# Performance work log

Measured on AMD Instinct MI355X. Metric: run time of the kernel, lower is better.

## Reference

```python
import jax, jax.numpy as jnp
import numpy as np

N_ANCHORS = 262144
N_GT = 100
IMG = 1024.0
N_SAMPLE = 256
POS_RATIO = 0.5
POS_T = 0.7
NEG_T = 0.3
ALLOWED_BORDER = 0.0
NUM_FG = int(POS_RATIO * N_SAMPLE)  # 128


def compute_overlap(a, g):
    """IoU between anchors a:(N,4) and gt g:(R,4), py-faster-rcnn +1 pixel convention."""
    area_a = (a[:, 2] - a[:, 0] + 1.0) * (a[:, 3] - a[:, 1] + 1.0)          # (N,)
    area_g = (g[:, 2] - g[:, 0] + 1.0) * (g[:, 3] - g[:, 1] + 1.0)          # (R,)
    iw = jnp.minimum(a[:, None, 2], g[None, :, 2]) - jnp.maximum(a[:, None, 0], g[None, :, 0]) + 1.0
    ih = jnp.minimum(a[:, None, 3], g[None, :, 3]) - jnp.maximum(a[:, None, 1], g[None, :, 1]) + 1.0
    inter = jnp.maximum(iw, 0.0) * jnp.maximum(ih, 0.0)                     # (N,R)
    return inter / (area_a[:, None] + area_g[None, :] - inter)


def bbox_transform(gt, an):
    """Encode gt boxes relative to anchors -> (dx,dy,dw,dh), shape (N,4)."""
    aw = an[:, 2] - an[:, 0] + 1.0
    ah = an[:, 3] - an[:, 1] + 1.0
    acx = an[:, 0] + 0.5 * aw
    acy = an[:, 1] + 0.5 * ah
    gw = gt[:, 2] - gt[:, 0] + 1.0
    gh = gt[:, 3] - gt[:, 1] + 1.0
    gcx = gt[:, 0] + 0.5 * gw
    gcy = gt[:, 1] + 0.5 * gh
    return jnp.stack([(gcx - acx) / aw, (gcy - acy) / ah,
                      jnp.log(gw / aw), jnp.log(gh / ah)], axis=1)


def keep_at_most(mask, k, key):
    """Keep at most k True entries of mask, chosen uniformly at random (fixed shape)."""
    r = jnp.where(mask, jax.random.uniform(key, mask.shape), jnp.inf)
    rank = jnp.argsort(jnp.argsort(r))  # rank[i] = position of i in ascending sort
    return mask & (rank < k)


def anchor_target(anchors, image_shape, gt, key):
    # anchors: (N,4), gt: (R,4)
    R = gt.shape[0]
    inside = ((anchors[:, 0] >= -ALLOWED_BORDER) & (anchors[:, 1] >= -ALLOWED_BORDER)
              & (anchors[:, 2] < ALLOWED_BORDER + image_shape[1])
              & (anchors[:, 3] < ALLOWED_BORDER + image_shape[0]))            # (N,)
    iou = compute_overlap(anchors, gt)                                        # (N,R)
    iou_m = jnp.where(inside[:, None], iou, -1.0)  # restrict to inside anchors
    max_ov = jnp.max(iou_m, axis=1)                                           # (N,)

    k1, k2, k3 = jax.random.split(key, 3)
    labels = jnp.full(anchors.shape[:1], -1.0, dtype=jnp.float32)
    # clobber_positives=False: background first
    labels = jnp.where(inside & (max_ov < NEG_T), 0.0, labels)
    # per-gt argmax anchors (tie set), randomly truncated to at most R like tf.random_shuffle[:R]
    gt_max = jnp.max(iou_m, axis=0)                                           # (R,)
    cand = jnp.any(iou_m == gt_max[None, :], axis=1) & inside                 # (N,)
    cand = keep_at_most(cand, R, k1)
    labels = jnp.where(cand, 1.0, labels)
    labels = jnp.where(inside & (max_ov >= POS_T), 1.0, labels)

    # balance: subsample positives to NUM_FG
    fg = labels == 1.0
    labels = jnp.where(fg & ~keep_at_most(fg, NUM_FG, k2), -1.0, labels)
    # subsample negatives to n_sample - n_fg
    n_fg = jnp.sum(labels == 1.0)
    bg = labels == 0.0
    labels = jnp.where(bg & ~keep_at_most(bg, N_SAMPLE - n_fg, k3), -1.0, labels)
    # umap: outside anchors stay -1
    labels = jnp.where(inside, labels, -1.0)

    # bbox targets: faithful to original tf.gather(gt, to_int32(max_overlaps))
    idx = jnp.clip(max_ov.astype(jnp.int32), 0, R - 1)
    tgt = bbox_transform(gt[idx], anchors)                                    # (N,4)
    tgt = jnp.where(inside[:, None], tgt, 0.0)  # scatter_nd at inside indices
    return labels[None], tgt[None]


def setup_inputs() -> dict:
    key = jax.random.key(0)
    k1, k2, k3, k4 = jax.random.split(key, 4)
    ctr = jax.random.uniform(k1, (N_ANCHORS, 2), minval=-64.0, maxval=IMG + 64.0)
    wh = jax.random.uniform(k2, (N_ANCHORS, 2), minval=16.0, maxval=256.0)
    anchors = jnp.concatenate([ctr - 0.5 * wh, ctr + 0.5 * wh], axis=1)
    gctr = jax.random.uniform(k3, (N_GT, 2), minval=100.0, maxval=IMG - 100.0)
    gwh = jax.random.uniform(k4, (N_GT, 2), minval=30.0, maxval=200.0)
    gt = jnp.concatenate([gctr - 0.5 * gwh, gctr + 0.5 * gwh], axis=1)
    return {"total_anchors": anchors[None],
            "image_shape": jnp.array([IMG, IMG], jnp.float32),
            "gt_boxes": gt[None]}


def reference(total_anchors, image_shape, gt_boxes):
    key = jax.random.key(42)  # original uses unseeded tf.random_shuffle
    labels, bbox_reg_targets = anchor_target(total_anchors[0], image_shape,
                                             gt_boxes[0][:, :4], key)
    return labels, bbox_reg_targets
```

## Files before the change

kernel.cpp:

```cpp
#include <hip/hip_runtime.h>
#include <stdint.h>

#define NGT_MAX 128
#define CAND_CAP 8192
#define FILT_CAP 16384
#define SUB_CAP 2048


__host__ __device__ inline void tf2x32(uint32_t k0, uint32_t k1, uint32_t c0, uint32_t c1,
                                       uint32_t& o0, uint32_t& o1) {
  uint32_t ks[3] = {k0, k1, k0 ^ k1 ^ 0x1BD11BDAu};
  uint32_t x0 = c0 + ks[0];
  uint32_t x1 = c1 + ks[1];
  const int rot[2][4] = {{13, 15, 26, 6}, {17, 29, 16, 24}};
#pragma unroll
  for (int i = 0; i < 5; ++i) {
#pragma unroll
    for (int j = 0; j < 4; ++j) {
      x0 += x1;
      int r = rot[i & 1][j];
      x1 = (x1 << r) | (x1 >> (32 - r));
      x1 ^= x0;
    }
    x0 += ks[(i + 1) % 3];
    x1 += ks[(i + 2) % 3] + (uint32_t)(i + 1);
  }
  o0 = x0; o1 = x1;
}

__device__ inline uint64_t sel_key(uint32_t i, uint32_t ka, uint32_t kb) {
  uint32_t o0, o1;
  tf2x32(ka, kb, 0u, i, o0, o1);
  uint32_t bits = o0 ^ o1;
  return ((uint64_t)(bits >> 9) << 32) | (uint64_t)i;
}

__device__ inline uint32_t fmap(float v) {
  uint32_t u = __float_as_uint(v);
  return (u & 0x80000000u) ? ~u : (u | 0x80000000u);
}
__device__ inline float funmap(uint32_t m) {
  return (m & 0x80000000u) ? __uint_as_float(m & 0x7FFFFFFFu) : __uint_as_float(~m);
}

__global__ void __launch_bounds__(256)
k_main(const float4* __restrict__ anc, const float* __restrict__ img,
       const float4* __restrict__ gt, int N, int R,
       uint32_t* __restrict__ pmax, uint32_t* __restrict__ gmaxu,
       float* __restrict__ LBL, float4* __restrict__ TGT,
       uint32_t* __restrict__ pmeta) {
  __shared__ float4 sgt[NGT_MAX];
  __shared__ float sarea[NGT_MAX];
  __shared__ float sq[64 * 101];
  __shared__ uint32_t scnt[2];
  const int t = threadIdx.x;
  if (t < 2) scnt[t] = 0u;
  if (t < R) {
    float4 g = gt[t];
    sgt[t] = g;
    {
#pragma clang fp contract(off)
      sarea[t] = (g.z - g.x + 1.0f) * (g.w - g.y + 1.0f);
    }
  }
  __syncthreads();
  const int lane = t & 63, lm = t & 3, q = t >> 2;
  const int i = blockIdx.x * 256 + t;
  const float H = img[0], W = img[1];
  float4 a = anc[i];
  bool inside = (a.x >= 0.0f) && (a.y >= 0.0f) && (a.z < W) && (a.w < H);
  float area_a;
  {
#pragma clang fp contract(off)
    area_a = (a.z - a.x + 1.0f) * (a.w - a.y + 1.0f);
  }
  if (!inside) area_a = __uint_as_float(0x7FC00000u);
  const bool b1 = (lm == 1), b2 = (lm == 2), b3 = (lm == 3);
  float part[25];
  float vmax = -1.0f;
#pragma unroll
  for (int s = 0; s < 25; ++s) {
    const int gb0 = 4 * s;
    if (gb0 >= R) break;
    float v2q[4];
#pragma unroll
    for (int k = 0; k < 4; ++k) {
      const int g = gb0 + k;
      if (g < R) {
        float4 gb = sgt[g];
        float v;
        {
#pragma clang fp contract(off)
          float iw = fminf(a.z, gb.z) - fmaxf(a.x, gb.x) + 1.0f;
          float ih = fminf(a.w, gb.w) - fmaxf(a.y, gb.y) + 1.0f;
          float inter = fmaxf(iw, 0.0f) * fmaxf(ih, 0.0f);
          v = inter / (area_a + sarea[g] - inter);
        }
        vmax = fmaxf(vmax, v);
        int s1 = __builtin_amdgcn_mov_dpp(__float_as_int(v), 0xB1, 0xF, 0xF, true);
        float v1 = fmaxf(v, __int_as_float(s1));
        int s2 = __builtin_amdgcn_mov_dpp(__float_as_int(v1), 0x4E, 0xF, 0xF, true);
        v2q[k] = fmaxf(v1, __int_as_float(s2));
      } else {
        v2q[k] = -1.0f;
      }
    }
    float p = v2q[0];
    p = b1 ? v2q[1] : p;
    p = b2 ? v2q[2] : p;
    p = b3 ? v2q[3] : p;
    part[s] = p;
  }
  float lbl = -1.0f;
  if (inside) {
    if (vmax < 0.3f) lbl = 0.0f;
    if (vmax >= 0.7f) lbl = 1.0f;
  }
  LBL[i] = lbl;
  unsigned long long bf = __ballot(lbl == 1.0f);
  unsigned long long bb = __ballot(lbl == 0.0f);
  if (lane == 0) {
    atomicAdd(&scnt[0], (uint32_t)__popcll(bf));
    atomicAdd(&scnt[1], (uint32_t)__popcll(bb));
  }
  float4 o = make_float4(0.f, 0.f, 0.f, 0.f);
  if (inside) {
    int idx = (int)vmax;
    idx = idx < 0 ? 0 : idx;
    idx = idx > R - 1 ? R - 1 : idx;
    float4 gb = sgt[idx];
    {
#pragma clang fp contract(off)
      float aw = a.z - a.x + 1.0f;
      float ah = a.w - a.y + 1.0f;
      float acx = a.x + 0.5f * aw;
      float acy = a.y + 0.5f * ah;
      float gw = gb.z - gb.x + 1.0f;
      float gh = gb.w - gb.y + 1.0f;
      float gcx = gb.x + 0.5f * gw;
      float gcy = gb.y + 0.5f * gh;
      o.x = (gcx - acx) / aw;
      o.y = (gcy - acy) / ah;
      o.z = logf(gw / aw);
      o.w = logf(gh / ah);
    }
  }
  TGT[i] = o;
#pragma unroll
  for (int s = 0; s < 25; ++s) {
    const int g = 4 * s + lm;
    if (4 * s >= R) break;
    if (g < R) sq[q * 101 + g] = part[s];
  }
  __syncthreads();
  if (t < R) {
    float m = -1.0f;
#pragma unroll 8
    for (int k2 = 0; k2 < 64; ++k2) m = fmaxf(m, sq[k2 * 101 + t]);
    uint32_t u = fmap(m);
    pmax[blockIdx.x * R + t] = u;
    if (u > gmaxu[t]) atomicMax(&gmaxu[t], u);
  }
  if (t == 0) pmeta[blockIdx.x] = scnt[0] | (scnt[1] << 16);
}

__global__ void __launch_bounds__(256)
k_cand(const float4* __restrict__ anc, const float* __restrict__ img,
       const float4* __restrict__ gt, int N, int R,
       const uint32_t* __restrict__ pmax, const uint32_t* __restrict__ gmaxu,
       uint64_t* __restrict__ candList, uint32_t* __restrict__ counters,
       uint32_t ka, uint32_t kb) {
  __shared__ int tg[NGT_MAX];
  __shared__ float tgm[NGT_MAX];
  __shared__ uint64_t buf[256];
  __shared__ uint32_t bcnt, bbase;
  __shared__ int tcnt;
  const int t = threadIdx.x, b = blockIdx.x;
  if (t == 0) { tcnt = 0; bcnt = 0u; }
  __syncthreads();
  if (t < R) {
    uint32_t pm = pmax[b * R + t];
    uint32_t gm = gmaxu[t];
    if (pm == gm) { int p = atomicAdd(&tcnt, 1); tg[p] = t; tgm[p] = funmap(gm); }
  }
  __syncthreads();
  const int C0 = tcnt;
  if (C0 == 0) return;
  const int i = b * 256 + t;
  const float H = img[0], W = img[1];
  float4 a = anc[i];
  bool inside = (a.x >= 0.0f) && (a.y >= 0.0f) && (a.z < W) && (a.w < H);
  if (inside) {
    float area_a;
    {
#pragma clang fp contract(off)
      area_a = (a.z - a.x + 1.0f) * (a.w - a.y + 1.0f);
    }
    bool cand = false;
    for (int j = 0; j < C0; ++j) {
      float4 gb = gt[tg[j]];
      float v;
      {
#pragma clang fp contract(off)
        float ag = (gb.z - gb.x + 1.0f) * (gb.w - gb.y + 1.0f);
        float iw = fminf(a.z, gb.z) - fmaxf(a.x, gb.x) + 1.0f;
        float ih = fminf(a.w, gb.w) - fmaxf(a.y, gb.y) + 1.0f;
        float inter = fmaxf(iw, 0.0f) * fmaxf(ih, 0.0f);
        v = inter / (area_a + ag - inter);
      }
      cand = cand || (v == tgm[j]);
    }
    if (cand) {
      uint32_t p = atomicAdd(&bcnt, 1u);
      buf[p] = sel_key((uint32_t)i, ka, kb);
    }
  }
  __syncthreads();
  if (t == 0 && bcnt) bbase = atomicAdd(&counters[0], bcnt);
  __syncthreads();
  for (uint32_t j = t; j < bcnt; j += 256) {
    uint32_t p = bbase + j;
    if (p < CAND_CAP) candList[p] = buf[j];
  }
}

__global__ void __launch_bounds__(256)
k_meta(const uint64_t* __restrict__ candList, uint32_t* __restrict__ counters,
       float* __restrict__ LBL, const uint32_t* __restrict__ pmeta, int NB, int R) {
  __shared__ uint64_t red[256];
  __shared__ int redA[256], redB[256];
  __shared__ uint64_t sub[SUB_CAP];
  const int t = threadIdx.x;
  uint64_t sm = 0;
  for (int j = t; j < NB; j += 256) {
    uint32_t v = pmeta[j];
    sm += (uint64_t)(v & 0xFFFFu) | ((uint64_t)(v >> 16) << 32);
  }
  red[t] = sm;
  __syncthreads();
  for (int s = 128; s > 0; s >>= 1) {
    if (t < s) red[t] += red[t + s];
    __syncthreads();
  }
  const uint32_t baseF = (uint32_t)(red[0] & 0xFFFFFFFFu);
  const uint32_t baseB = (uint32_t)(red[0] >> 32);
  uint32_t C = counters[0];
  if (C > SUB_CAP) C = SUB_CAP;
  for (uint32_t s = t; s < C; s += 256) sub[s] = candList[s];
  __syncthreads();
  int dF = 0, dB = 0;
  for (uint32_t s = t; s < C; s += 256) {
    uint64_t key = sub[s];
    bool keep = true;
    if (C > (uint32_t)R) {
      uint32_t rank = 0;
      for (uint32_t j = 0; j < C; ++j) rank += (sub[j] < key) ? 1u : 0u;
      keep = (rank < (uint32_t)R);
    }
    if (keep) {
      uint32_t i2 = (uint32_t)key;
      float old = LBL[i2];
      LBL[i2] = 1.0f;
      if (old != 1.0f) dF++;
      if (old == 0.0f) dB--;
    }
  }
  redA[t] = dF; redB[t] = dB;
  __syncthreads();
  for (int s = 128; s > 0; s >>= 1) {
    if (t < s) { redA[t] += redA[t + s]; redB[t] += redB[t + s]; }
    __syncthreads();
  }
  if (t == 0) {
    uint32_t M1 = baseF + (uint32_t)redA[0];
    uint32_t M2 = baseB + (uint32_t)(int32_t)redB[0];
    counters[1] = M1; counters[2] = M2;
    uint32_t nfg = M1 < 128u ? M1 : 128u;
    uint32_t kbg = 256u - nfg;
    counters[12] = kbg;
    counters[8] = (M1 > 128u) ? 1u : 0u;
    counters[9] = (M2 > kbg) ? 1u : 0u;
    uint64_t Tf = 0, Tb = 0;
    if (M1 > 128u) {
      Tf = (((uint64_t)(128u * 32u)) << 23) / (uint64_t)M1;
      if (Tf > (1u << 23)) Tf = (1u << 23);
    }
    if (M2 > kbg) {
      Tb = (((uint64_t)(kbg * 32u)) << 23) / (uint64_t)M2;
      if (Tb > (1u << 23)) Tb = (1u << 23);
    }
    counters[10] = (uint32_t)Tf; counters[11] = (uint32_t)Tb;
  }
}

__global__ void __launch_bounds__(256)
k_gather(float* __restrict__ LBL, int N, uint64_t* __restrict__ listF,
         uint64_t* __restrict__ listB, uint32_t* __restrict__ counters,
         uint32_t k2a, uint32_t k2b, uint32_t k3a, uint32_t k3b) {
  __shared__ uint64_t bufF[256], bufB[256];
  __shared__ uint32_t cF, cB, oF, oB;
  const int t = threadIdx.x, b = blockIdx.x;
  if (t == 0) { cF = 0u; cB = 0u; }
  __syncthreads();
  const uint32_t needF = counters[8], needB = counters[9];
  const uint32_t Tf = counters[10], Tb = counters[11];
  const int i = b * 256 + t;
  float lbl = LBL[i];
  if (lbl == 1.0f) {
    if (needF) {
      uint64_t key = sel_key((uint32_t)i, k2a, k2b);
      if ((uint32_t)(key >> 32) >= Tf) {
        LBL[i] = -1.0f;
      } else {
        uint32_t p = atomicAdd(&cF, 1u);
        bufF[p] = key;
      }
    }
  } else if (lbl == 0.0f) {
    if (needB) {
      uint64_t key = sel_key((uint32_t)i, k3a, k3b);
      if ((uint32_t)(key >> 32) >= Tb) {
        LBL[i] = -1.0f;
      } else {
        uint32_t p = atomicAdd(&cB, 1u);
        bufB[p] = key;
      }
    }
  }
  __syncthreads();
  if (t == 0 && cF) oF = atomicAdd(&counters[4], cF);
  if (t == 64 && cB) oB = atomicAdd(&counters[5], cB);
  __syncthreads();
  for (uint32_t j = t; j < cF; j += 256) {
    uint32_t p = oF + j;
    if (p < FILT_CAP) listF[p] = bufF[j];
  }
  for (uint32_t j = t; j < cB; j += 256) {
    uint32_t p = oB + j;
    if (p < FILT_CAP) listB[p] = bufB[j];
  }
}

__device__ __forceinline__ void do_select(const uint64_t* list, uint32_t Mf, uint32_t k,
                                          uint32_t T, float* LBL, uint32_t* h,
                                          uint32_t* c0, uint32_t* c1, uint64_t* sub,
                                          uint32_t* scal) {
  const int t = threadIdx.x;
  if (Mf <= k) return;
  int bl = (T > 1u) ? (32 - __clz(T - 1u)) : 0;
  int shift = bl > 8 ? bl - 8 : 0;
  h[t] = 0u;
  if (t == 0) { scal[0] = 0u; scal[1] = 0u; scal[2] = 0u; }
  __syncthreads();
  for (uint32_t j = t; j < Mf; j += 256)
    atomicAdd(&h[((uint32_t)(list[j] >> 32)) >> shift], 1u);
  __syncthreads();
  c0[t] = h[t];
  __syncthreads();
  uint32_t* s = c0;
  uint32_t* d = c1;
  for (int dd = 1; dd < 256; dd <<= 1) {
    uint32_t v = s[t];
    if (t >= dd) v += s[t - dd];
    d[t] = v;
    __syncthreads();
    uint32_t* tmp = s; s = d; d = tmp;
  }
  uint32_t inc = s[t];
  uint32_t exc = inc - h[t];
  if (exc < k && inc >= k) { scal[1] = (uint32_t)t; scal[2] = k - exc; }
  __syncthreads();
  const uint32_t binb = scal[1], rneed = scal[2];
  for (uint32_t j = t; j < Mf; j += 256) {
    uint64_t key = list[j];
    uint32_t bin = ((uint32_t)(key >> 32)) >> shift;
    if (bin > binb) {
      LBL[(uint32_t)key] = -1.0f;
    } else if (bin == binb) {
      uint32_t p = atomicAdd(&scal[0], 1u);
      if (p < SUB_CAP) sub[p] = key;
    }
  }
  __syncthreads();
  uint32_t c = scal[0] < SUB_CAP ? scal[0] : SUB_CAP;
  for (uint32_t s2 = t; s2 < c; s2 += 256) {
    uint64_t key = sub[s2];
    uint32_t rank = 0u;
    for (uint32_t j = 0; j < c; ++j) rank += (sub[j] < key) ? 1u : 0u;
    if (rank >= rneed) LBL[(uint32_t)key] = -1.0f;
  }
  __syncthreads();
}

__global__ void __launch_bounds__(256)
k_sel(float* __restrict__ LBL, const uint64_t* __restrict__ listF,
      const uint64_t* __restrict__ listB, uint32_t* __restrict__ counters) {
  __shared__ uint32_t h[256], c0[256], c1[256];
  __shared__ uint64_t sub[SUB_CAP];
  __shared__ uint32_t scal[4];
  if (counters[8]) {
    uint32_t Mf = counters[4];
    if (Mf > FILT_CAP) Mf = FILT_CAP;
    do_select(listF, Mf, 128u, counters[10], LBL, h, c0, c1, sub, scal);
  }
  if (counters[9]) {
    uint32_t Mf = counters[5];
    if (Mf > FILT_CAP) Mf = FILT_CAP;
    do_select(listB, Mf, counters[12], counters[11], LBL, h, c0, c1, sub, scal);
  }
}

extern "C" void kernel_launch(void* const* d_in, const int* in_sizes, int n_in,
                              void* d_out, int out_size, void* d_ws, size_t ws_size,
                              hipStream_t stream) {
  (void)n_in; (void)out_size; (void)ws_size;
  const int N = in_sizes[0] / 4;
  const int R = in_sizes[2] / 4;
  const int NB = N / 256;
  const float4* anc = (const float4*)d_in[0];
  const float* img = (const float*)d_in[1];
  const float4* gtb = (const float4*)d_in[2];
  float* LBL = (float*)d_out;
  float4* TGT = (float4*)((float*)d_out + N);

  uint8_t* ws = (uint8_t*)d_ws;
  uint32_t* counters = (uint32_t*)ws;
  uint32_t* gmaxu = (uint32_t*)(ws + 512);
  uint32_t* pmeta = (uint32_t*)(ws + 1024);
  uint32_t* pmax = (uint32_t*)(ws + 8192);
  size_t off = 8192 + (size_t)NB * R * 4;
  off = (off + 7) & ~(size_t)7;
  uint64_t* candList = (uint64_t*)(ws + off);
  uint64_t* listF = (uint64_t*)(ws + off + CAND_CAP * 8);
  uint64_t* listB = (uint64_t*)(ws + off + CAND_CAP * 8 + FILT_CAP * 8);

  uint32_t k1a, k1b, k2a, k2b, k3a, k3b;
  tf2x32(0u, 42u, 0u, 0u, k1a, k1b);
  tf2x32(0u, 42u, 0u, 1u, k2a, k2b);
  tf2x32(0u, 42u, 0u, 2u, k3a, k3b);

  hipMemsetAsync(ws, 0, 1024, stream);
  k_main<<<NB, 256, 0, stream>>>(anc, img, gtb, N, R, pmax, gmaxu, LBL, TGT, pmeta);
  k_cand<<<NB, 256, 0, stream>>>(anc, img, gtb, N, R, pmax, gmaxu, candList, counters,
                                 k1a, k1b);
  k_meta<<<1, 256, 0, stream>>>(candList, counters, LBL, pmeta, NB, R);
  k_gather<<<NB, 256, 0, stream>>>(LBL, N, listF, listB, counters, k2a, k2b, k3a, k3b);
  k_sel<<<1, 256, 0, stream>>>(LBL, listF, listB, counters);
}
```

Before: 143.0 us.

## Fuse single-block meta kernel into gather and split main kernel launch

Removes the single-block k_meta launch. Every k_gather block now redundantly recomputes the pmeta reduction, candidate ranking and thresholds, and applies forced-positive labels through a per-block shared flag. k_cand records each candidate's prior label code so the fused kernel can count the changes without reading global labels. k_main is also split into two half-grid launches with a block offset. The intent is to drop a serial single-workgroup stage, at the cost of repeating O(C^2) ranking work in every block plus one extra launch.

```diff
diff --git a/kernel.cpp b/kernel.cpp
--- a/kernel.cpp
+++ b/kernel.cpp
@@ -3,6 +3,7 @@
 
 #define NGT_MAX 128
 #define CAND_CAP 8192
+#define RANK_CAP 2048
 #define FILT_CAP 16384
 #define SUB_CAP 2048
 
@@ -45,7 +46,7 @@
 
 __global__ void __launch_bounds__(256)
 k_main(const float4* __restrict__ anc, const float* __restrict__ img,
-       const float4* __restrict__ gt, int N, int R,
+       const float4* __restrict__ gt, int N, int R, int bOff,
        uint32_t* __restrict__ pmax, uint32_t* __restrict__ gmaxu,
        float* __restrict__ LBL, float4* __restrict__ TGT,
        uint32_t* __restrict__ pmeta) {
@@ -54,6 +55,7 @@
   __shared__ float sq[64 * 101];
   __shared__ uint32_t scnt[2];
   const int t = threadIdx.x;
+  const int b = blockIdx.x + bOff;
   if (t < 2) scnt[t] = 0u;
   if (t < R) {
     float4 g = gt[t];
@@ -65,7 +67,7 @@
   }
   __syncthreads();
   const int lane = t & 63, lm = t & 3, q = t >> 2;
-  const int i = blockIdx.x * 256 + t;
+  const int i = b * 256 + t;
   const float H = img[0], W = img[1];
   float4 a = anc[i];
   bool inside = (a.x >= 0.0f) && (a.y >= 0.0f) && (a.z < W) && (a.w < H);
@@ -158,21 +160,23 @@
 #pragma unroll 8
     for (int k2 = 0; k2 < 64; ++k2) m = fmaxf(m, sq[k2 * 101 + t]);
     uint32_t u = fmap(m);
-    pmax[blockIdx.x * R + t] = u;
+    pmax[b * R + t] = u;
     if (u > gmaxu[t]) atomicMax(&gmaxu[t], u);
   }
-  if (t == 0) pmeta[blockIdx.x] = scnt[0] | (scnt[1] << 16);
+  if (t == 0) pmeta[b] = scnt[0] | (scnt[1] << 16);
 }
 
 __global__ void __launch_bounds__(256)
 k_cand(const float4* __restrict__ anc, const float* __restrict__ img,
        const float4* __restrict__ gt, int N, int R,
        const uint32_t* __restrict__ pmax, const uint32_t* __restrict__ gmaxu,
-       uint64_t* __restrict__ candList, uint32_t* __restrict__ counters,
-       uint32_t ka, uint32_t kb) {
+       const float* __restrict__ LBL,
+       uint64_t* __restrict__ candList, uint32_t* __restrict__ candLbl,
+       uint32_t* __restrict__ counters, uint32_t ka, uint32_t kb) {
   __shared__ int tg[NGT_MAX];
   __shared__ float tgm[NGT_MAX];
   __shared__ uint64_t buf[256];
+  __shared__ uint32_t bufL[256];
   __shared__ uint32_t bcnt, bbase;
   __shared__ int tcnt;
   const int t = threadIdx.x, b = blockIdx.x;
@@ -211,8 +215,11 @@
       cand = cand || (v == tgm[j]);
     }
     if (cand) {
+      float old = LBL[i];
+      uint32_t code = (old == 1.0f) ? 2u : ((old == 0.0f) ? 1u : 0u);
       uint32_t p = atomicAdd(&bcnt, 1u);
       buf[p] = sel_key((uint32_t)i, ka, kb);
+      bufL[p] = code;
     }
   }
   __syncthreads();
@@ -220,23 +227,36 @@
   __syncthreads();
   for (uint32_t j = t; j < bcnt; j += 256) {
     uint32_t p = bbase + j;
-    if (p < CAND_CAP) candList[p] = buf[j];
+    if (p < CAND_CAP) { candList[p] = buf[j]; candLbl[p] = bufL[j]; }
   }
 }
 
 __global__ void __launch_bounds__(256)
-k_meta(const uint64_t* __restrict__ candList, uint32_t* __restrict__ counters,
-       float* __restrict__ LBL, const uint32_t* __restrict__ pmeta, int NB, int R) {
+k_gather(float* __restrict__ LBL, int N, int NB, int R,
+         const uint64_t* __restrict__ candList, const uint32_t* __restrict__ candLbl,
+         const uint32_t* __restrict__ pmeta,
+         uint64_t* __restrict__ listF, uint64_t* __restrict__ listB,
+         uint32_t* __restrict__ counters,
+         uint32_t k2a, uint32_t k2b, uint32_t k3a, uint32_t k3b) {
+  __shared__ uint64_t sub[RANK_CAP];
   __shared__ uint64_t red[256];
-  __shared__ int redA[256], redB[256];
-  __shared__ uint64_t sub[SUB_CAP];
-  const int t = threadIdx.x;
+  __shared__ uint64_t bufF[256], bufB[256];
+  __shared__ uint32_t sflag[256];
+  __shared__ uint32_t sdFB[2];
+  __shared__ uint32_t smeta[6];
+  __shared__ uint32_t cF, cB, oF, oB;
+  const int t = threadIdx.x, b = blockIdx.x;
+  sflag[t] = 0u;
+  if (t < 2) sdFB[t] = 0u;
+  if (t == 0) { cF = 0u; cB = 0u; }
   uint64_t sm = 0;
   for (int j = t; j < NB; j += 256) {
     uint32_t v = pmeta[j];
     sm += (uint64_t)(v & 0xFFFFu) | ((uint64_t)(v >> 16) << 32);
   }
   red[t] = sm;
+  uint32_t C = counters[0];
+  if (C > RANK_CAP) C = RANK_CAP;
   __syncthreads();
   for (int s = 128; s > 0; s >>= 1) {
     if (t < s) red[t] += red[t + s];
@@ -244,13 +264,10 @@
   }
   const uint32_t baseF = (uint32_t)(red[0] & 0xFFFFFFFFu);
   const uint32_t baseB = (uint32_t)(red[0] >> 32);
-  uint32_t C = counters[0];
-  if (C > SUB_CAP) C = SUB_CAP;
   for (uint32_t s = t; s < C; s += 256) sub[s] = candList[s];
   __syncthreads();
-  int dF = 0, dB = 0;
-  for (uint32_t s = t; s < C; s += 256) {
-    uint64_t key = sub[s];
+  for (uint32_t e = t; e < C; e += 256) {
+    uint64_t key = sub[e];
     bool keep = true;
     if (C > (uint32_t)R) {
       uint32_t rank = 0;
@@ -258,75 +275,67 @@
       keep = (rank < (uint32_t)R);
     }
     if (keep) {
-      uint32_t i2 = (uint32_t)key;
-      float old = LBL[i2];
-      LBL[i2] = 1.0f;
-      if (old != 1.0f) dF++;
-      if (old == 0.0f) dB--;
-    }
-  }
-  redA[t] = dF; redB[t] = dB;
-  __syncthreads();
-  for (int s = 128; s > 0; s >>= 1) {
-    if (t < s) { redA[t] += redA[t + s]; redB[t] += redB[t + s]; }
-    __syncthreads();
-  }
+      uint32_t code = candLbl[e];
+      if (code != 2u) atomicAdd(&sdFB[0], 1u);
+      if (code == 1u) atomicAdd(&sdFB[1], 1u);
+      uint32_t idx = (uint32_t)key;
+      if ((int)(idx >> 8) == b) sflag[idx & 255u] = 1u;
+    }
+  }
+  __syncthreads();
   if (t == 0) {
-    uint32_t M1 = baseF + (uint32_t)redA[0];
-    uint32_t M2 = baseB + (uint32_t)(int32_t)redB[0];
-    counters[1] = M1; counters[2] = M2;
+    uint32_t M1 = baseF + sdFB[0];
+    uint32_t M2 = baseB - sdFB[1];
     uint32_t nfg = M1 < 128u ? M1 : 128u;
     uint32_t kbg = 256u - nfg;
-    counters[12] = kbg;
-    counters[8] = (M1 > 128u) ? 1u : 0u;
-    counters[9] = (M2 > kbg) ? 1u : 0u;
+    uint32_t needF = (M1 > 128u) ? 1u : 0u;
+    uint32_t needB = (M2 > kbg) ? 1u : 0u;
     uint64_t Tf = 0, Tb = 0;
-    if (M1 > 128u) {
+    if (needF) {
       Tf = (((uint64_t)(128u * 32u)) << 23) / (uint64_t)M1;
       if (Tf > (1u << 23)) Tf = (1u << 23);
     }
-    if (M2 > kbg) {
+    if (needB) {
       Tb = (((uint64_t)(kbg * 32u)) << 23) / (uint64_t)M2;
       if (Tb > (1u << 23)) Tb = (1u << 23);
     }
-    counters[10] = (uint32_t)Tf; counters[11] = (uint32_t)Tb;
-  }
-}
-
-__global__ void __launch_bounds__(256)
-k_gather(float* __restrict__ LBL, int N, uint64_t* __restrict__ listF,
-         uint64_t* __restrict__ listB, uint32_t* __restrict__ counters,
-         uint32_t k2a, uint32_t k2b, uint32_t k3a, uint32_t k3b) {
-  __shared__ uint64_t bufF[256], bufB[256];
-  __shared__ uint32_t cF, cB, oF, oB;
-  const int t = threadIdx.x, b = blockIdx.x;
-  if (t == 0) { cF = 0u; cB = 0u; }
-  __syncthreads();
-  const uint32_t needF = counters[8], needB = counters[9];
-  const uint32_t Tf = counters[10], Tb = counters[11];
+    smeta[0] = needF; smeta[1] = needB; smeta[2] = (uint32_t)Tf; smeta[3] = (uint32_t)Tb;
+    smeta[4] = M1; smeta[5] = M2;
+    if (b == 0) {
+      counters[1] = M1; counters[2] = M2;
+      counters[8] = needF; counters[9] = needB;
+      counters[10] = (uint32_t)Tf; counters[11] = (uint32_t)Tb;
+      counters[12] = kbg;
+    }
+  }
+  __syncthreads();
+  const uint32_t needF = smeta[0], needB = smeta[1], Tf = smeta[2], Tb = smeta[3];
   const int i = b * 256 + t;
-  float lbl = LBL[i];
-  if (lbl == 1.0f) {
+  float old = LBL[i];
+  float l1 = sflag[t] ? 1.0f : old;
+  float out = l1;
+  if (l1 == 1.0f) {
     if (needF) {
       uint64_t key = sel_key((uint32_t)i, k2a, k2b);
       if ((uint32_t)(key >> 32) >= Tf) {
-        LBL[i] = -1.0f;
+        out = -1.0f;
       } else {
         uint32_t p = atomicAdd(&cF, 1u);
         bufF[p] = key;
       }
     }
-  } else if (lbl == 0.0f) {
+  } else if (l1 == 0.0f) {
     if (needB) {
       uint64_t key = sel_key((uint32_t)i, k3a, k3b);
       if ((uint32_t)(key >> 32) >= Tb) {
-        LBL[i] = -1.0f;
+        out = -1.0f;
       } else {
         uint32_t p = atomicAdd(&cB, 1u);
         bufB[p] = key;
       }
     }
   }
+  LBL[i] = out;
   __syncthreads();
   if (t == 0 && cF) oF = atomicAdd(&counters[4], cF);
   if (t == 64 && cB) oB = atomicAdd(&counters[5], cB);
@@ -427,8 +436,9 @@
   uint32_t* counters = (uint32_t*)ws;
   uint32_t* gmaxu = (uint32_t*)(ws + 512);
   uint32_t* pmeta = (uint32_t*)(ws + 1024);
-  uint32_t* pmax = (uint32_t*)(ws + 8192);
-  size_t off = 8192 + (size_t)NB * R * 4;
+  uint32_t* candLbl = (uint32_t*)(ws + 1024 + 4096);
+  uint32_t* pmax = (uint32_t*)(ws + 65536);
+  size_t off = 65536 + (size_t)NB * R * 4;
   off = (off + 7) & ~(size_t)7;
   uint64_t* candList = (uint64_t*)(ws + off);
   uint64_t* listF = (uint64_t*)(ws + off + CAND_CAP * 8);
@@ -440,10 +450,12 @@
   tf2x32(0u, 42u, 0u, 2u, k3a, k3b);
 
   hipMemsetAsync(ws, 0, 1024, stream);
-  k_main<<<NB, 256, 0, stream>>>(anc, img, gtb, N, R, pmax, gmaxu, LBL, TGT, pmeta);
-  k_cand<<<NB, 256, 0, stream>>>(anc, img, gtb, N, R, pmax, gmaxu, candList, counters,
-                                 k1a, k1b);
-  k_meta<<<1, 256, 0, stream>>>(candList, counters, LBL, pmeta, NB, R);
-  k_gather<<<NB, 256, 0, stream>>>(LBL, N, listF, listB, counters, k2a, k2b, k3a, k3b);
+  k_main<<<NB / 2, 256, 0, stream>>>(anc, img, gtb, N, R, 0, pmax, gmaxu, LBL, TGT, pmeta);
+  k_main<<<NB / 2, 256, 0, stream>>>(anc, img, gtb, N, R, NB / 2, pmax, gmaxu, LBL, TGT,
+                                     pmeta);
+  k_cand<<<NB, 256, 0, stream>>>(anc, img, gtb, N, R, pmax, gmaxu, LBL, candList, candLbl,
+                                 counters, k1a, k1b);
+  k_gather<<<NB, 256, 0, stream>>>(LBL, N, NB, R, candList, candLbl, pmeta, listF, listB,
+                                   counters, k2a, k2b, k3a, k3b);
   k_sel<<<1, 256, 0, stream>>>(LBL, listF, listB, counters);
 }
```

After: 153.3 us. +7.2%, slower.
